# Performance work log

Measured on AMD Instinct MI355X. Metric: run time of the kernel, lower is better.

## Reference

```python
import jax, jax.numpy as jnp
import numpy as np

B, C, D, H, W = 1, 32, 48, 64, 208
EPS = 1e-5  # BatchNorm eps


def setup_inputs() -> dict:
    key = jax.random.key(0)
    ks = jax.random.split(key, 8)
    x = jax.random.normal(ks[0], (B, C, D, H, W), jnp.float32)
    g = jax.random.normal(ks[1], (B, 20, H, W), jnp.float32)
    conv_w = jax.random.normal(ks[2], (C, C, 3, 3, 3), jnp.float32) * 0.02
    bn1_gamma = 1.0 + 0.1 * jax.random.normal(ks[3], (C,), jnp.float32)
    bn1_beta = 0.1 * jax.random.normal(ks[4], (C,), jnp.float32)
    bn1_mean = 0.1 * jax.random.normal(ks[5], (C,), jnp.float32)
    bn1_var = jax.random.uniform(ks[6], (C,), jnp.float32, 0.5, 1.5)
    bn2_gamma = 1.0 + 0.1 * jax.random.normal(ks[7], (C,), jnp.float32)
    bn2_beta = jnp.zeros((C,), jnp.float32)
    bn2_mean = jnp.zeros((C,), jnp.float32)
    bn2_var = jnp.ones((C,), jnp.float32)
    return {
        'x': x, 'g': g, 'conv_w': conv_w,
        'bn1_gamma': bn1_gamma, 'bn1_beta': bn1_beta, 'bn1_mean': bn1_mean, 'bn1_var': bn1_var,
        'bn2_gamma': bn2_gamma, 'bn2_beta': bn2_beta, 'bn2_mean': bn2_mean, 'bn2_var': bn2_var,
    }


def _l1_normalize(k):
    # F.normalize(k, p=1, dim=1)
    return k / jnp.maximum(jnp.sum(jnp.abs(k), axis=1, keepdims=True), 1e-12)


def _sga_scan(x, w):
    """Directional semi-global aggregation along the LAST axis.
    x: [B,C,D,H,L] cost volume, w: [B,5,H,L] L1-normalized guidance weights.
    Recurrence (GANet SGA):
      A[p,d] = w0*x[p,d] + w1*A[p-1,d] + w2*A[p-1,d-1] + w3*A[p-1,d+1] + w4*max_d' A[p-1,d']
    """
    xs = jnp.moveaxis(x, -1, 0)  # [L,B,C,D,H]
    ws = jnp.moveaxis(w, -1, 0)  # [L,B,5,H]

    def step(prev, inp):
        xi, wi = inp  # [B,C,D,H], [B,5,H]
        w0, w1, w2, w3, w4 = [wi[:, i][:, None, None, :] for i in range(5)]
        up = jnp.concatenate([prev[:, :, :1], prev[:, :, :-1]], axis=2)   # A[d-1]
        dn = jnp.concatenate([prev[:, :, 1:], prev[:, :, -1:]], axis=2)   # A[d+1]
        mx = jnp.max(prev, axis=2, keepdims=True)                          # max_d A
        out = w0 * xi + w1 * prev + w2 * up + w3 * dn + w4 * mx
        return out, out

    _, outs = jax.lax.scan(step, xs[0], (xs, ws))  # boundary: carry init = raw cost slice
    return jnp.moveaxis(outs, 0, -1)


def _sga(x, k1, k2, k3, k4):
    # direction 1: left -> right (along W)
    d1 = _sga_scan(x, k1)
    # direction 2: right -> left
    d2 = jnp.flip(_sga_scan(jnp.flip(x, -1), jnp.flip(k2, -1)), -1)
    # vertical directions: swap H<->W so the scan axis is H
    xv = jnp.swapaxes(x, 3, 4)  # [B,C,D,W,H]
    d3 = jnp.swapaxes(_sga_scan(xv, jnp.swapaxes(k3, 2, 3)), 3, 4)  # top -> bottom
    d4 = jnp.swapaxes(
        jnp.flip(_sga_scan(jnp.flip(xv, -1), jnp.flip(jnp.swapaxes(k4, 2, 3), -1)), -1), 3, 4)
    # GANet combines directions with an elementwise max
    return jnp.maximum(jnp.maximum(d1, d2), jnp.maximum(d3, d4))


def _bn3d(x, gamma, beta, mean, var):
    s = (gamma / jnp.sqrt(var + EPS))[None, :, None, None, None]
    return (x - mean[None, :, None, None, None]) * s + beta[None, :, None, None, None]


def _conv3d_same(x, w):
    return jax.lax.conv_general_dilated(
        x, w, window_strides=(1, 1, 1), padding=[(1, 1)] * 3,
        dimension_numbers=('NCDHW', 'OIDHW', 'NCDHW'))


def reference(x, g, conv_w, bn1_gamma, bn1_beta, bn1_mean, bn1_var,
              bn2_gamma, bn2_beta, bn2_mean, bn2_var):
    rem = x
    k1, k2, k3, k4 = jnp.split(g, 4, axis=1)  # each [B,5,H,W]
    k1, k2, k3, k4 = map(_l1_normalize, (k1, k2, k3, k4))
    a = _sga(x, k1, k2, k3, k4)
    # refine=True branch: BN+ReLU then BasicConv(3x3x3, BN, no relu)
    a = jax.nn.relu(_bn3d(a, bn1_gamma, bn1_beta, bn1_mean, bn1_var))
    a = _conv3d_same(a, conv_w)
    a = _bn3d(a, bn2_gamma, bn2_beta, bn2_mean, bn2_var)
    return jax.nn.relu(a + rem)
```

## Files before the change

kernel.cpp:

```cpp
#include <hip/hip_runtime.h>
#include <hip/hip_bf16.h>
#include <cstddef>

#define C_ 32
#define D_ 48
#define H_ 64
#define W_ 208
#define WP_ 210
#define HW_ 13312
#define HS_ 9984
#define EPS_ 1e-5f

typedef __attribute__((ext_vector_type(8))) short short8;
typedef __attribute__((ext_vector_type(4))) float float4v;
typedef __attribute__((ext_vector_type(16))) float float16v;
typedef __attribute__((ext_vector_type(2))) __fp16 half2v;

template<int CTRL>
__device__ __forceinline__ float dppmov(float x) {
    int v = __builtin_bit_cast(int, x);
    return __builtin_bit_cast(float,
        __builtin_amdgcn_update_dpp(v, v, CTRL, 0xf, 0xf, false));
}
template<int CTRL>
__device__ __forceinline__ float dppmax(float m) {
    return fmaxf(m, dppmov<CTRL>(m));
}
__device__ __forceinline__ float rl(float v, int idx) {
    return __builtin_bit_cast(float,
        __builtin_amdgcn_readlane(__builtin_bit_cast(int, v), idx));
}

__device__ __forceinline__ float sga_step_dpp(float A, float xi,
    float w0, float w1, float w2, float w3, float w4, bool actv, bool ge47)
{
    float up = dppmov<0x138>(A);
    float dn = dppmov<0x130>(A);
    dn = ge47 ? A : dn;
    float m = actv ? A : -3.4e38f;
    m = dppmax<0x111>(m);
    m = dppmax<0x112>(m);
    m = dppmax<0x114>(m);
    m = dppmax<0x118>(m);
    m = dppmax<0x142>(m);
    m = dppmax<0x143>(m);
    float mall = rl(m, 63);
    return (w0*xi + w1*A) + ((w2*up + w3*dn) + w4*mall);
}

__global__ __launch_bounds__(256) void prep_kernel(
    const float* __restrict__ g, const float* __restrict__ cw,
    float* __restrict__ wn, float* __restrict__ wnT,
    __hip_bfloat16* __restrict__ wrep, unsigned* __restrict__ actu)
{
    int idx = blockIdx.x * 256 + threadIdx.x;
    if (idx < 4 * HW_) {
        int dir = idx / HW_;
        int hw  = idx % HW_;
        const float* gb = g + dir * 5 * HW_ + hw;
        float v0 = gb[0*HW_], v1 = gb[1*HW_], v2 = gb[2*HW_], v3 = gb[3*HW_], v4 = gb[4*HW_];
        float s = fabsf(v0)+fabsf(v1)+fabsf(v2)+fabsf(v3)+fabsf(v4);
        float inv = 1.0f / fmaxf(s, 1e-12f);
        v0 *= inv; v1 *= inv; v2 *= inv; v3 *= inv; v4 *= inv;
        float* ob = wn + dir * 5 * HW_ + hw;
        ob[0*HW_] = v0; ob[1*HW_] = v1; ob[2*HW_] = v2; ob[3*HW_] = v3; ob[4*HW_] = v4;
        if (dir >= 2) {
            int hq = hw / W_, wq = hw % W_;
            float* oT = wnT + ((size_t)((dir-2)*5)*W_ + wq)*H_ + hq;
            oT[0]       = v0; oT[1*HW_] = v1; oT[2*HW_] = v2;
            oT[3*HW_]   = v3; oT[4*HW_] = v4;
        }
    } else if (idx < 4 * HW_ + 27 * 2 * 64 * 8) {
        int j = idx - 4 * HW_;
        int e    = j & 7;
        int lane = (j >> 3) & 63;
        int q    = j >> 9;
        int cih  = q & 1;
        int tap  = q >> 1;
        int co = lane & 31;
        int ci = cih * 16 + (lane >> 5) * 8 + e;
        wrep[j] = __float2bfloat16(cw[(co * C_ + ci) * 27 + tap]);
    } else {
        int j2 = idx - (4 * HW_ + 27648);
        int hd  = j2 >> 5;
        int r   = j2 & 31;
        int col = (r >> 4) ? 209 : 0;
        int cu  = r & 15;
        actu[((size_t)hd * WP_ + col) * 16 + cu] = 0u;
    }
}

__global__ __launch_bounds__(256) void t0_kernel(
    const float* __restrict__ x, __hip_bfloat16* __restrict__ xt)
{
    __shared__ float t[48 * 257];
    int tid = threadIdx.x;
    int c  = blockIdx.x / 52;
    int q0 = (blockIdx.x % 52) * 256;
    #pragma unroll
    for (int dd = 0; dd < 48; ++dd)
        t[dd * 257 + tid] = x[((size_t)c * 48 + dd) * HW_ + q0 + tid];
    __syncthreads();
    unsigned* xtu = (unsigned*)xt;
    #pragma unroll
    for (int k = 0; k < 24; ++k) {
        int f = tid + 256 * k;
        int d2 = f % 24, hwl = f / 24;
        union { unsigned u; __hip_bfloat16 hh[2]; } pk;
        pk.hh[0] = __float2bfloat16(t[(2 * d2) * 257 + hwl]);
        pk.hh[1] = __float2bfloat16(t[(2 * d2 + 1) * 257 + hwl]);
        xtu[(((size_t)c * HW_ + q0 + hwl) * 48 + 2 * d2) >> 1] = pk.u;
    }
}

template<int LN>
__device__ __forceinline__ float chunk_fwd(float A,
    const __hip_bfloat16* __restrict__ xp, __hip_bfloat16* __restrict__ dp,
    const float* __restrict__ wb, int P0, int lane, bool actv, bool ge47)
{
    float xr[LN];
    #pragma unroll
    for (int j = 0; j < LN; ++j) xr[j] = __bfloat162float(xp[(size_t)(P0 + j) * 48]);
    int lm = lane & (LN - 1);
    float wv0 = wb[0*HW_ + P0 + lm], wv1 = wb[1*HW_ + P0 + lm],
          wv2 = wb[2*HW_ + P0 + lm], wv3 = wb[3*HW_ + P0 + lm],
          wv4 = wb[4*HW_ + P0 + lm];
    #pragma unroll
    for (int j = 0; j < LN; ++j) {
        A = sga_step_dpp(A, xr[j], rl(wv0,j), rl(wv1,j), rl(wv2,j),
                         rl(wv3,j), rl(wv4,j), actv, ge47);
        if (actv) dp[(size_t)(P0 + j) * 48] = __float2bfloat16(A);
    }
    return A;
}

template<int LN>
__device__ __forceinline__ float chunk_rev(float A,
    const __hip_bfloat16* __restrict__ xp, __hip_bfloat16* __restrict__ dp,
    const float* __restrict__ wb, int P0, int lane, bool actv, bool ge47)
{
    float xr[LN]; __hip_bfloat16 dr[LN];
    #pragma unroll
    for (int j = 0; j < LN; ++j) {
        xr[j] = __bfloat162float(xp[(size_t)(P0 + j) * 48]);
        dr[j] = dp[(size_t)(P0 + j) * 48];
    }
    int lm = lane & (LN - 1);
    float wv0 = wb[0*HW_ + P0 + lm], wv1 = wb[1*HW_ + P0 + lm],
          wv2 = wb[2*HW_ + P0 + lm], wv3 = wb[3*HW_ + P0 + lm],
          wv4 = wb[4*HW_ + P0 + lm];
    #pragma unroll
    for (int j = LN - 1; j >= 0; --j) {
        A = sga_step_dpp(A, xr[j], rl(wv0,j), rl(wv1,j), rl(wv2,j),
                         rl(wv3,j), rl(wv4,j), actv, ge47);
        if (actv)
            dp[(size_t)(P0 + j) * 48] =
                __float2bfloat16(fmaxf(__bfloat162float(dr[j]), A));
    }
    return A;
}

__global__ __launch_bounds__(256) void sga_w_kernel(
    const __hip_bfloat16* __restrict__ xt, const float* __restrict__ wn,
    __hip_bfloat16* __restrict__ d12)
{
    int lane = threadIdx.x & 63;
    int wid  = blockIdx.x * 4 + (threadIdx.x >> 6);
    int c = wid >> 6, h = wid & 63;
    int d = lane < 48 ? lane : 47;
    bool actv = lane < 48, ge47 = lane >= 47;
    const __hip_bfloat16* xp = xt + ((size_t)c * HW_ + h * W_) * 48 + d;
    __hip_bfloat16* dp = d12 + ((size_t)c * HW_ + h * W_) * 48 + d;
    const float* w1 = wn + (size_t)0 * 5 * HW_ + h * W_;
    const float* w2 = wn + (size_t)1 * 5 * HW_ + h * W_;

    float A = __bfloat162float(xp[0]);
    for (int cc = 0; cc < 6; ++cc)
        A = chunk_fwd<32>(A, xp, dp, w1, cc * 32, lane, actv, ge47);
    A = chunk_fwd<16>(A, xp, dp, w1, 192, lane, actv, ge47);

    A = __bfloat162float(xp[(size_t)207 * 48]);
    A = chunk_rev<16>(A, xp, dp, w2, 192, lane, actv, ge47);
    for (int cc = 0; cc < 6; ++cc)
        A = chunk_rev<32>(A, xp, dp, w2, 160 - cc * 32, lane, actv, ge47);
}

__global__ __launch_bounds__(256, 6) void sga_h_kernel(
    const __hip_bfloat16* __restrict__ xt, const float* __restrict__ wnT,
    __hip_bfloat16* __restrict__ d12,
    const float* __restrict__ g1, const float* __restrict__ b1,
    const float* __restrict__ m1, const float* __restrict__ v1)
{
    __shared__ __fp16 sA[2][2][64][48];

    int lane = threadIdx.x & 63;
    int widb = threadIdx.x >> 6;
    int colb = widb >> 1;
    int dir  = widb & 1;
    int gcol = blockIdx.x * 2 + colb;
    int c = gcol / W_, w = gcol % W_;
    int d = lane < 48 ? lane : 47;
    bool actv = lane < 48, ge47 = lane >= 47;
    const __hip_bfloat16* xp = xt + ((size_t)c * HW_ + w) * 48 + d;
    const float* wb = wnT + ((size_t)(dir * 5) * W_ + w) * H_;
    int il = lane >> 3, jl = lane & 7;
    bool wact = il < 5;

    float xb[3][8];
    float wAr[3];

    if (dir == 0) {
        #pragma unroll
        for (int j = 0; j < 8; ++j) {
            xb[0][j] = __bfloat162float(xp[(size_t)j * HS_]);
            xb[1][j] = __bfloat162float(xp[(size_t)(8 + j) * HS_]);
        }
        wAr[0] = wact ? wb[il * HW_ + jl] : 0.0f;
        wAr[1] = wact ? wb[il * HW_ + 8 + jl] : 0.0f;
        float A = xb[0][0];
        #pragma unroll
        for (int cc = 0; cc < 8; ++cc) {
            const int buf = cc % 3;
            if (cc < 6) {
                const int nb = (cc + 2) % 3;
                #pragma unroll
                for (int j = 0; j < 8; ++j)
                    xb[nb][j] = __bfloat162float(xp[(size_t)((cc + 2) * 8 + j) * HS_]);
                wAr[nb] = wact ? wb[il * HW_ + (cc + 2) * 8 + jl] : 0.0f;
            }
            #pragma unroll
            for (int j = 0; j < 8; ++j) {
                A = sga_step_dpp(A, xb[buf][j], rl(wAr[buf], j), rl(wAr[buf], 8 + j),
                                 rl(wAr[buf], 16 + j), rl(wAr[buf], 24 + j),
                                 rl(wAr[buf], 32 + j), actv, ge47);
                if (actv) sA[colb][0][cc * 8 + j][d] = (__fp16)A;
            }
        }
    } else {
        #pragma unroll
        for (int j = 0; j < 8; ++j) {
            xb[0][j] = __bfloat162float(xp[(size_t)(56 + j) * HS_]);
            xb[1][j] = __bfloat162float(xp[(size_t)(48 + j) * HS_]);
        }
        wAr[0] = wact ? wb[il * HW_ + 56 + jl] : 0.0f;
        wAr[1] = wact ? wb[il * HW_ + 48 + jl] : 0.0f;
        float A = xb[0][7];
        #pragma unroll
        for (int cc2 = 0; cc2 < 8; ++cc2) {
            const int cc = 7 - cc2;
            const int buf = cc2 % 3;
            if (cc2 < 6) {
                const int nb = (cc2 + 2) % 3;
                #pragma unroll
                for (int j = 0; j < 8; ++j)
                    xb[nb][j] = __bfloat162float(xp[(size_t)((cc - 2) * 8 + j) * HS_]);
                wAr[nb] = wact ? wb[il * HW_ + (cc - 2) * 8 + jl] : 0.0f;
            }
            #pragma unroll
            for (int j = 7; j >= 0; --j) {
                A = sga_step_dpp(A, xb[buf][j], rl(wAr[buf], j), rl(wAr[buf], 8 + j),
                                 rl(wAr[buf], 16 + j), rl(wAr[buf], 24 + j),
                                 rl(wAr[buf], 32 + j), actv, ge47);
                if (actv) sA[colb][1][cc * 8 + j][d] = (__fp16)A;
            }
        }
    }

    __syncthreads();

    float s1 = g1[c] * rsqrtf(v1[c] + EPS_);
    float o1 = b1[c] - m1[c] * s1;
    __hip_bfloat16* dp = d12 + ((size_t)c * HW_ + w) * 48 + d;
    #pragma unroll
    for (int t = 0; t < 32; ++t) {
        int h = dir * 32 + t;
        float dv = __bfloat162float(dp[(size_t)h * HS_]);
        float d3 = (float)sA[colb][0][h][d];
        float d4 = (float)sA[colb][1][h][d];
        float comb = fmaxf(fmaxf(d3, d4), dv);
        if (actv)
            dp[(size_t)h * HS_] = __float2bfloat16(fmaxf(comb * s1 + o1, 0.0f));
    }
}

__global__ __launch_bounds__(256) void trans_kernel(
    const __hip_bfloat16* __restrict__ st, __hip_bfloat16* __restrict__ act)
{
    __shared__ float t[8 * 1571];
    int tid = threadIdx.x;
    int h  = blockIdx.x / 26;
    int w0 = (blockIdx.x % 26) * 8;
    const unsigned* stu = (const unsigned*)st;
    #pragma unroll
    for (int k = 0; k < 24; ++k) {
        int f = tid + 256 * k;
        int d2 = f % 24, wl = (f / 24) % 8, c = f / 192;
        unsigned u = stu[(((size_t)c * HW_ + h * W_ + w0 + wl) * 48 + 2 * d2) >> 1];
        const __hip_bfloat16* bp = (const __hip_bfloat16*)&u;
        t[wl * 1571 + c * 49 + 2 * d2]     = __bfloat162float(bp[0]);
        t[wl * 1571 + c * 49 + 2 * d2 + 1] = __bfloat162float(bp[1]);
    }
    __syncthreads();
    unsigned* actu = (unsigned*)act;
    #pragma unroll
    for (int k = 0; k < 24; ++k) {
        int f = tid + 256 * k;
        int cp = f % 16, wl = (f / 16) % 8, d = f / 128;
        union { unsigned u; __hip_bfloat16 hh[2]; } pk;
        pk.hh[0] = __float2bfloat16(t[wl * 1571 + (2 * cp) * 49 + d]);
        pk.hh[1] = __float2bfloat16(t[wl * 1571 + (2 * cp + 1) * 49 + d]);
        actu[(((size_t)h * 48 + d) * WP_ + w0 + wl + 1) * 16 + cp] = pk.u;
    }
}

__global__ __launch_bounds__(256, 3) void conv_kernel(
    const __hip_bfloat16* __restrict__ act,
    const short8* __restrict__ wrep,
    const float* __restrict__ x,
    const float* __restrict__ g2, const float* __restrict__ b2,
    const float* __restrict__ m2, const float* __restrict__ v2,
    float* __restrict__ out)
{
    int lane = threadIdx.x & 63;
    int wid  = __builtin_amdgcn_readfirstlane(blockIdx.x * 4 + (threadIdx.x >> 6));
    int wt = wid % 7;
    int t1 = wid / 7;
    int h  = t1 & 63;
    int d0 = (t1 >> 6) * 4;
    int w0 = wt * 32;
    int n   = lane & 31;
    int ci0 = (lane >> 5) * 8;

    float16v acc0 = (float16v)(0.0f);
    float16v acc1 = (float16v)(0.0f);
    float16v acc2 = (float16v)(0.0f);
    float16v acc3 = (float16v)(0.0f);

    #pragma unroll
    for (int kh = 0; kh < 3; ++kh) {
        int hh = h + kh - 1;
        if (hh < 0 || hh >= H_) continue;
        #pragma unroll
        for (int kw = 0; kw < 3; ++kw) {
            int wwp = w0 + kw + n;
            wwp = wwp < 209 ? wwp : 209;
            const __hip_bfloat16* pl =
                act + ((size_t)hh * D_ * WP_ + wwp) * C_ + ci0
                    + (ptrdiff_t)(d0 - 1) * WP_ * C_;
            #pragma unroll
            for (int cih = 0; cih < 2; ++cih) {
                const __hip_bfloat16* pc = pl + cih * 16;
                short8 af[3];
                #pragma unroll
                for (int kd = 0; kd < 3; ++kd)
                    af[kd] = wrep[(((kd*3 + kh)*3 + kw)*2 + cih)*64 + lane];
                short8 bf[6];
                #pragma unroll
                for (int p = 0; p < 6; ++p) {
                    int dd = d0 - 1 + p;
                    if (dd >= 0 && dd < D_) {
                        bf[p] = *(const short8*)(pc + (ptrdiff_t)p * WP_ * C_);
                    } else {
                        short8 z = {0,0,0,0,0,0,0,0};
                        bf[p] = z;
                    }
                }
                #pragma unroll
                for (int kd = 0; kd < 3; ++kd) {
                    acc0 = __builtin_amdgcn_mfma_f32_32x32x16_bf16(af[kd], bf[kd+0], acc0, 0, 0, 0);
                    acc1 = __builtin_amdgcn_mfma_f32_32x32x16_bf16(af[kd], bf[kd+1], acc1, 0, 0, 0);
                    acc2 = __builtin_amdgcn_mfma_f32_32x32x16_bf16(af[kd], bf[kd+2], acc2, 0, 0, 0);
                    acc3 = __builtin_amdgcn_mfma_f32_32x32x16_bf16(af[kd], bf[kd+3], acc3, 0, 0, 0);
                }
            }
        }
    }

    int wl = w0 + n;
    bool wvalid = wl < W_;
    int coh = 4 * (lane >> 5);
    #pragma unroll
    for (int r = 0; r < 16; ++r) {
        int co = (r & 3) + 8 * (r >> 2) + coh;
        float s2 = g2[co] * rsqrtf(v2[co] + EPS_);
        float o2 = b2[co] - m2[co] * s2;
        size_t idx0 = ((size_t)(co * D_ + d0) * H_ + h) * W_ + wl;
        if (wvalid) {
            out[idx0]           = fmaxf(acc0[r] * s2 + o2 + x[idx0],           0.0f);
            out[idx0 + HW_]     = fmaxf(acc1[r] * s2 + o2 + x[idx0 + HW_],     0.0f);
            out[idx0 + 2*HW_]   = fmaxf(acc2[r] * s2 + o2 + x[idx0 + 2*HW_],   0.0f);
            out[idx0 + 3*HW_]   = fmaxf(acc3[r] * s2 + o2 + x[idx0 + 3*HW_],   0.0f);
        }
    }
}

extern "C" void kernel_launch(void* const* d_in, const int* in_sizes, int n_in,
                              void* d_out, int out_size, void* d_ws, size_t ws_size,
                              hipStream_t stream)
{
    const float* x    = (const float*)d_in[0];
    const float* g    = (const float*)d_in[1];
    const float* cw   = (const float*)d_in[2];
    const float* bn1g = (const float*)d_in[3];
    const float* bn1b = (const float*)d_in[4];
    const float* bn1m = (const float*)d_in[5];
    const float* bn1v = (const float*)d_in[6];
    const float* bn2g = (const float*)d_in[7];
    const float* bn2b = (const float*)d_in[8];
    const float* bn2m = (const float*)d_in[9];
    const float* bn2v = (const float*)d_in[10];
    float* out = (float*)d_out;

    char* ws = (char*)d_ws;
    float* wn  = (float*)ws;
    float* wnT = (float*)(ws + 1064960);
    __hip_bfloat16* wrep = (__hip_bfloat16*)(ws + 1597440);
    __hip_bfloat16* d12t = (__hip_bfloat16*)(ws + 1652736);
    __hip_bfloat16* act  = (__hip_bfloat16*)(ws + 42547200);
    __hip_bfloat16* xt = (__hip_bfloat16*)out;

    prep_kernel<<<700, 256, 0, stream>>>(g, cw, wn, wnT, wrep, (unsigned*)act);
    t0_kernel<<<1664, 256, 0, stream>>>(x, xt);
    sga_w_kernel<<<512, 256, 0, stream>>>(xt, wn, d12t);
    sga_h_kernel<<<3328, 256, 0, stream>>>(xt, wnT, d12t, bn1g, bn1b, bn1m, bn1v);
    trans_kernel<<<1664, 256, 0, stream>>>(d12t, act);
    conv_kernel<<<1344, 256, 0, stream>>>(act, (const short8*)wrep, x,
                                          bn2g, bn2b, bn2m, bn2v, out);
}
```

Baseline: 443.4 us.

## Stage conv input tiles in LDS with depth-padded activation layout

```diff
diff --git a/kernel.cpp b/kernel.cpp
--- a/kernel.cpp
+++ b/kernel.cpp
@@ -4,6 +4,7 @@
 
 #define C_ 32
 #define D_ 48
+#define DP_ 50
 #define H_ 64
 #define W_ 208
 #define WP_ 210
@@ -70,7 +71,7 @@
             oT[0]       = v0; oT[1*HW_] = v1; oT[2*HW_] = v2;
             oT[3*HW_]   = v3; oT[4*HW_] = v4;
         }
-    } else if (idx < 4 * HW_ + 27 * 2 * 64 * 8) {
+    } else if (idx < 4 * HW_ + 27648) {
         int j = idx - 4 * HW_;
         int e    = j & 7;
         int lane = (j >> 3) & 63;
@@ -80,13 +81,22 @@
         int co = lane & 31;
         int ci = cih * 16 + (lane >> 5) * 8 + e;
         wrep[j] = __float2bfloat16(cw[(co * C_ + ci) * 27 + tap]);
-    } else {
+    } else if (idx < 4 * HW_ + 27648 + 98304) {
         int j2 = idx - (4 * HW_ + 27648);
         int hd  = j2 >> 5;
         int r   = j2 & 31;
         int col = (r >> 4) ? 209 : 0;
         int cu  = r & 15;
-        actu[((size_t)hd * WP_ + col) * 16 + cu] = 0u;
+        int h = hd / 48, dd = hd % 48;
+        actu[(((size_t)h * DP_ + dd + 1) * WP_ + col) * 16 + cu] = 0u;
+    } else {
+        int j3 = idx - (4 * HW_ + 27648 + 98304);
+        int pl   = j3 >= 215040;
+        int r3   = pl ? j3 - 215040 : j3;
+        int h    = r3 / 3360;
+        int rest = r3 % 3360;
+        int dpad = pl ? (DP_ - 1) : 0;
+        actu[((size_t)h * DP_ + dpad) * WP_ * 16 + rest] = 0u;
     }
 }
 
@@ -309,11 +319,11 @@
         union { unsigned u; __hip_bfloat16 hh[2]; } pk;
         pk.hh[0] = __float2bfloat16(t[wl * 1571 + (2 * cp) * 49 + d]);
         pk.hh[1] = __float2bfloat16(t[wl * 1571 + (2 * cp + 1) * 49 + d]);
-        actu[(((size_t)h * 48 + d) * WP_ + w0 + wl + 1) * 16 + cp] = pk.u;
-    }
-}
-
-__global__ __launch_bounds__(256, 3) void conv_kernel(
+        actu[(((size_t)h * DP_ + d + 1) * WP_ + w0 + wl + 1) * 16 + cp] = pk.u;
+    }
+}
+
+__global__ __launch_bounds__(256, 4) void conv_kernel(
     const __hip_bfloat16* __restrict__ act,
     const short8* __restrict__ wrep,
     const float* __restrict__ x,
@@ -321,64 +331,69 @@
     const float* __restrict__ m2, const float* __restrict__ v2,
     float* __restrict__ out)
 {
-    int lane = threadIdx.x & 63;
-    int wid  = __builtin_amdgcn_readfirstlane(blockIdx.x * 4 + (threadIdx.x >> 6));
-    int wt = wid % 7;
-    int t1 = wid / 7;
-    int h  = t1 & 63;
-    int d0 = (t1 >> 6) * 4;
-    int w0 = wt * 32;
-    int n   = lane & 31;
-    int ci0 = (lane >> 5) * 8;
+    __shared__ __hip_bfloat16 sAct[10 * 34 * 40];
+
+    int tid  = threadIdx.x;
+    int lane = tid & 63;
+    int v    = tid >> 6;
+    int bid  = blockIdx.x;
+    int wt   = bid % 7;
+    int t    = bid / 7;
+    int h    = t & 63;
+    int d0b  = (t >> 6) * 8;
+    int w0   = wt * 32;
+    int n    = lane & 31;
+    int half = lane >> 5;
 
     float16v acc0 = (float16v)(0.0f);
     float16v acc1 = (float16v)(0.0f);
-    float16v acc2 = (float16v)(0.0f);
-    float16v acc3 = (float16v)(0.0f);
+
+    const short8* ap8 = (const short8*)act;
 
     #pragma unroll
     for (int kh = 0; kh < 3; ++kh) {
         int hh = h + kh - 1;
         if (hh < 0 || hh >= H_) continue;
+        __syncthreads();
+        #pragma unroll
+        for (int k = 0; k < 6; ++k) {
+            int i = tid + 256 * k;
+            if (i < 1360) {
+                int dp = i / 136;
+                int r  = i - dp * 136;
+                int wl = r >> 2, q = r & 3;
+                int wc = w0 + wl; wc = wc < 209 ? wc : 209;
+                short8 vd = ap8[(((size_t)hh * DP_ + d0b + dp) * WP_ + wc) * 4 + q];
+                *(short8*)&sAct[(dp * 34 + wl) * 40 + q * 8] = vd;
+            }
+        }
+        __syncthreads();
         #pragma unroll
         for (int kw = 0; kw < 3; ++kw) {
-            int wwp = w0 + kw + n;
-            wwp = wwp < 209 ? wwp : 209;
-            const __hip_bfloat16* pl =
-                act + ((size_t)hh * D_ * WP_ + wwp) * C_ + ci0
-                    + (ptrdiff_t)(d0 - 1) * WP_ * C_;
             #pragma unroll
             for (int cih = 0; cih < 2; ++cih) {
-                const __hip_bfloat16* pc = pl + cih * 16;
                 short8 af[3];
                 #pragma unroll
                 for (int kd = 0; kd < 3; ++kd)
                     af[kd] = wrep[(((kd*3 + kh)*3 + kw)*2 + cih)*64 + lane];
-                short8 bf[6];
+                short8 bf[4];
                 #pragma unroll
-                for (int p = 0; p < 6; ++p) {
-                    int dd = d0 - 1 + p;
-                    if (dd >= 0 && dd < D_) {
-                        bf[p] = *(const short8*)(pc + (ptrdiff_t)p * WP_ * C_);
-                    } else {
-                        short8 z = {0,0,0,0,0,0,0,0};
-                        bf[p] = z;
-                    }
-                }
+                for (int p = 0; p < 4; ++p)
+                    bf[p] = *(const short8*)
+                        &sAct[((2*v + p) * 34 + kw + n) * 40 + cih * 16 + half * 8];
                 #pragma unroll
                 for (int kd = 0; kd < 3; ++kd) {
-                    acc0 = __builtin_amdgcn_mfma_f32_32x32x16_bf16(af[kd], bf[kd+0], acc0, 0, 0, 0);
+                    acc0 = __builtin_amdgcn_mfma_f32_32x32x16_bf16(af[kd], bf[kd],   acc0, 0, 0, 0);
                     acc1 = __builtin_amdgcn_mfma_f32_32x32x16_bf16(af[kd], bf[kd+1], acc1, 0, 0, 0);
-                    acc2 = __builtin_amdgcn_mfma_f32_32x32x16_bf16(af[kd], bf[kd+2], acc2, 0, 0, 0);
-                    acc3 = __builtin_amdgcn_mfma_f32_32x32x16_bf16(af[kd], bf[kd+3], acc3, 0, 0, 0);
                 }
             }
         }
     }
 
+    int d0 = d0b + 2 * v;
     int wl = w0 + n;
     bool wvalid = wl < W_;
-    int coh = 4 * (lane >> 5);
+    int coh = 4 * half;
     #pragma unroll
     for (int r = 0; r < 16; ++r) {
         int co = (r & 3) + 8 * (r >> 2) + coh;
@@ -386,10 +401,8 @@
         float o2 = b2[co] - m2[co] * s2;
         size_t idx0 = ((size_t)(co * D_ + d0) * H_ + h) * W_ + wl;
         if (wvalid) {
-            out[idx0]           = fmaxf(acc0[r] * s2 + o2 + x[idx0],           0.0f);
-            out[idx0 + HW_]     = fmaxf(acc1[r] * s2 + o2 + x[idx0 + HW_],     0.0f);
-            out[idx0 + 2*HW_]   = fmaxf(acc2[r] * s2 + o2 + x[idx0 + 2*HW_],   0.0f);
-            out[idx0 + 3*HW_]   = fmaxf(acc3[r] * s2 + o2 + x[idx0 + 3*HW_],   0.0f);
+            out[idx0]       = fmaxf(acc0[r] * s2 + o2 + x[idx0],       0.0f);
+            out[idx0 + HW_] = fmaxf(acc1[r] * s2 + o2 + x[idx0 + HW_], 0.0f);
         }
     }
 }
@@ -419,11 +432,11 @@
     __hip_bfloat16* act  = (__hip_bfloat16*)(ws + 42547200);
     __hip_bfloat16* xt = (__hip_bfloat16*)out;
 
-    prep_kernel<<<700, 256, 0, stream>>>(g, cw, wn, wnT, wrep, (unsigned*)act);
+    prep_kernel<<<2380, 256, 0, stream>>>(g, cw, wn, wnT, wrep, (unsigned*)act);
     t0_kernel<<<1664, 256, 0, stream>>>(x, xt);
     sga_w_kernel<<<512, 256, 0, stream>>>(xt, wn, d12t);
     sga_h_kernel<<<3328, 256, 0, stream>>>(xt, wnT, d12t, bn1g, bn1b, bn1m, bn1v);
     trans_kernel<<<1664, 256, 0, stream>>>(d12t, act);
-    conv_kernel<<<1344, 256, 0, stream>>>(act, (const short8*)wrep, x,
+    conv_kernel<<<2688, 256, 0, stream>>>(act, (const short8*)wrep, x,
                                           bn2g, bn2b, bn2m, bn2v, out);
 }
```

After: 415.7 us. 6.3% less time.
